# Kernel tuning notes

Measured on AMD Instinct MI355X. Metric: run time of the kernel, lower is better.

The kernel has to match this reference:

```python
import jax, jax.numpy as jnp
import numpy as np

ROPE_BASE = 100.0


def _rope1d(tok, pos):
    # tok: [B, H, N, d], pos: [B, N] int. Matches croco apply_rope1d.
    d = tok.shape[-1]
    inv_freq = 1.0 / (ROPE_BASE ** (jnp.arange(0, d, 2, dtype=jnp.float32) / d))  # [d/2]
    ang = pos[:, None, :, None].astype(jnp.float32) * inv_freq  # [B,1,N,d/2]
    ang = jnp.concatenate([ang, ang], axis=-1)  # [B,1,N,d]
    cos, sin = jnp.cos(ang).astype(tok.dtype), jnp.sin(ang).astype(tok.dtype)
    x1, x2 = tok[..., : d // 2], tok[..., d // 2 :]
    rot = jnp.concatenate([-x2, x1], axis=-1)  # rotate_half
    return tok * cos + rot * sin


def _rope2d(tok, pos):
    # tok: [B, H, N, D]; first half of D uses pos[...,0] (y), second half pos[...,1] (x)
    y, x = jnp.split(tok, 2, axis=-1)
    return jnp.concatenate([_rope1d(y, pos[..., 0]), _rope1d(x, pos[..., 1])], axis=-1)


def setup_inputs() -> dict:
    key = jax.random.key(0)
    ks = jax.random.split(key, 10)
    B, N, C = 8, 1024, 768
    s = 0.02
    return {
        "query": jax.random.normal(ks[0], (B, N, C), jnp.float32),
        "key": jax.random.normal(ks[1], (B, N, C), jnp.float32),
        "value": jax.random.normal(ks[2], (B, N, C), jnp.float32),
        "qpos": jax.random.randint(ks[3], (B, N, 2), 0, 32, jnp.int32),
        "kpos": jax.random.randint(ks[4], (B, N, 2), 0, 32, jnp.int32),
        "Wq": jax.random.normal(ks[5], (C, C), jnp.float32) * s,
        "Wk": jax.random.normal(ks[6], (C, C), jnp.float32) * s,
        "Wv": jax.random.normal(ks[7], (C, C), jnp.float32) * s,
        "Wo": jax.random.normal(ks[8], (C, C), jnp.float32) * s,
        "bo": jnp.zeros((C,), jnp.float32),
    }


def reference(query, key, value, qpos, kpos, Wq, Wk, Wv, Wo, bo):
    B, Nq, C = query.shape
    H = 12
    hd = C // H
    scale = hd ** -0.5
    # projections (torch Linear: x @ W^T), then split heads -> [B,H,N,hd]
    q = jnp.einsum("bnc,dc->bnd", query, Wq).reshape(B, Nq, H, hd).transpose(0, 2, 1, 3)
    k = jnp.einsum("bnc,dc->bnd", key, Wk).reshape(B, -1, H, hd).transpose(0, 2, 1, 3)
    v = jnp.einsum("bnc,dc->bnd", value, Wv).reshape(B, -1, H, hd).transpose(0, 2, 1, 3)
    q = _rope2d(q, qpos)
    k = _rope2d(k, kpos)
    attn = jnp.einsum("bhqd,bhkd->bhqk", q, k) * scale
    attn = jax.nn.softmax(attn, axis=-1)
    x = jnp.einsum("bhqk,bhkd->bhqd", attn, v)
    x = x.transpose(0, 2, 1, 3).reshape(B, Nq, C)
    return jnp.einsum("bnc,dc->bnd", x, Wo) + bo
```

## Files before the change

kernel.cpp:

```cpp
#include <hip/hip_runtime.h>
#include <hip/hip_bf16.h>
#include <hip/hip_fp16.h>

#define B_DIM 8
#define N_DIM 1024
#define C_DIM 768
#define H_DIM 12
#define HD    64
#define M_DIM (B_DIM * N_DIM)
#define BH    (B_DIM * H_DIM)

static constexpr size_t TEN = (size_t)M_DIM * C_DIM;
static constexpr size_t WN  = (size_t)C_DIM * C_DIM;

typedef __attribute__((ext_vector_type(8))) short    s16x8;
typedef __attribute__((ext_vector_type(8))) _Float16 f16x8;
typedef __attribute__((ext_vector_type(4))) float    f32x4;

__device__ __forceinline__ unsigned short f2h(float f) {
    __half h = __float2half(f);
    return __half_as_ushort(h);
}


__global__ __launch_bounds__(256)
void convX(const float* __restrict__ q, const float* __restrict__ k,
           const float* __restrict__ v, unsigned short* __restrict__ XS)
{
    const int t  = blockIdx.z;
    const int p  = blockIdx.y;
    const int kb = blockIdx.x;
    const float* src = (t == 0) ? q : (t == 1 ? k : v);
    unsigned short* dst = XS + (size_t)t * TEN;

    const int mr = threadIdx.x & 127;
    const int gh = threadIdx.x >> 7;
    const float* s = src + ((size_t)(p * 128 + mr)) * C_DIM + kb * 32 + gh * 16;
    float4 v0 = *(const float4*)(s);
    float4 v1 = *(const float4*)(s + 4);
    float4 v2 = *(const float4*)(s + 8);
    float4 v3 = *(const float4*)(s + 12);
    float f[16] = {v0.x,v0.y,v0.z,v0.w, v1.x,v1.y,v1.z,v1.w,
                   v2.x,v2.y,v2.z,v2.w, v3.x,v3.y,v3.z,v3.w};
    #pragma unroll
    for (int gj = 0; gj < 2; ++gj) {
        int gg = gh * 2 + gj;
        s16x8 h8;
        #pragma unroll
        for (int e = 0; e < 8; ++e)
            h8[e] = (short)f2h(f[gj * 8 + e]);
        size_t a = ((((size_t)p * 24 + kb) * 4 + gg) * 128 + mr) * 8;
        *(s16x8*)(dst + a) = h8;
    }
}

__global__ __launch_bounds__(256)
void convW(const float* __restrict__ wq, const float* __restrict__ wk,
           const float* __restrict__ wv, const float* __restrict__ wo,
           unsigned short* __restrict__ WS)
{
    const int t  = blockIdx.z;
    const int p  = blockIdx.y;
    const int kb = blockIdx.x;
    const float* src = (t == 0) ? wq : (t == 1 ? wk : (t == 2 ? wv : wo));
    unsigned short* dst = WS + (size_t)t * WN;

    const int mr = threadIdx.x & 127;
    const int gh = threadIdx.x >> 7;
    const float* s = src + ((size_t)(p * 128 + mr)) * C_DIM + kb * 32 + gh * 16;
    float4 v0 = *(const float4*)(s);
    float4 v1 = *(const float4*)(s + 4);
    float4 v2 = *(const float4*)(s + 8);
    float4 v3 = *(const float4*)(s + 12);
    float f[16] = {v0.x,v0.y,v0.z,v0.w, v1.x,v1.y,v1.z,v1.w,
                   v2.x,v2.y,v2.z,v2.w, v3.x,v3.y,v3.z,v3.w};
    #pragma unroll
    for (int gj = 0; gj < 2; ++gj) {
        int gg = gh * 2 + gj;
        s16x8 h8;
        #pragma unroll
        for (int e = 0; e < 8; ++e)
            h8[e] = (short)f2h(f[gj * 8 + e]);
        size_t a = ((((size_t)p * 24 + kb) * 4 + gg) * 128 + mr) * 8;
        *(s16x8*)(dst + a) = h8;
    }
}

__global__ void angles512(float2* __restrict__ tab)
{
    int t = threadIdx.x;
    int pos = t >> 4, j = t & 15;
    float ang = (float)pos * exp2f(-(float)j * 0.41524101186092029f);
    float s, c;
    sincosf(ang, &s, &c);
    tab[t] = make_float2(c, s);
}

template<int MODE>
__global__ __launch_bounds__(256)
void gemmF(const unsigned short* __restrict__ XQ, const unsigned short* __restrict__ XK,
           const unsigned short* __restrict__ XV,
           const unsigned short* __restrict__ WQ, const unsigned short* __restrict__ WK,
           const unsigned short* __restrict__ WV,
           const int* __restrict__ qpos, const int* __restrict__ kpos,
           const float2* __restrict__ tab,
           unsigned short* __restrict__ OQ, unsigned short* __restrict__ OK_,
           unsigned short* __restrict__ OV,
           const float* __restrict__ bias, float* __restrict__ Of)
{
    __shared__ unsigned short sA[3][4][128][8];
    __shared__ unsigned short sB[3][4][128][8];

    const int tid  = threadIdx.x;
    const int lane = tid & 63;
    const int w    = tid >> 6;
    const int wr   = w >> 1, wc = w & 1;
    const int c    = lane & 15, g = lane >> 4;

    const int chunk = gridDim.x >> 3;
    const int wgid  = (blockIdx.x & 7) * chunk + (blockIdx.x >> 3);
    int z, m0, n0;
    if (MODE == 1) {
        z = wgid / 384;
        int r = wgid - z * 384;
        m0 = (r / 6) * 128;
        n0 = (r % 6) * 128;
    } else {
        z = 0;
        m0 = (wgid / 6) * 128;
        n0 = (wgid % 6) * 128;
    }

    const unsigned short *Ap, *Bp;
    if (MODE == 0 || z == 0) { Ap = XQ; Bp = WQ; }
    else if (z == 1)         { Ap = XK; Bp = WK; }
    else                     { Ap = XV; Bp = WV; }

    const size_t abase0 = (size_t)(m0 >> 7) * 24 * 4096;
    const size_t bbase0 = (size_t)(n0 >> 7) * 24 * 4096;

    f32x4 acc[4][4] = {};

    auto stage = [&](int kb, int buf) {
        #pragma unroll
        for (int t = 0; t < 4; ++t) {
            int is = w * 4 + t;
            int sel = is >> 3;
            int j   = is & 7;
            int gg  = j >> 1, half = j & 1;
            const unsigned short* srcp =
                (sel ? Bp + bbase0 : Ap + abase0) + (size_t)kb * 4096
                + (size_t)gg * 1024 + (half * 64 + lane) * 8;
            unsigned short* dstp = sel ? &sB[buf][gg][half * 64][0]
                                       : &sA[buf][gg][half * 64][0];
            __builtin_amdgcn_global_load_lds(
                (const __attribute__((address_space(1))) void*)srcp,
                (__attribute__((address_space(3))) void*)dstp,
                16, 0, 0);
        }
    };

    stage(0, 0);
    stage(1, 1);
    stage(2, 2);

    for (int kb = 0; kb < 24; ++kb) {
        int buf = kb % 3;
        if (kb < 22)      asm volatile("s_waitcnt vmcnt(8)" ::: "memory");
        else if (kb == 22) asm volatile("s_waitcnt vmcnt(4)" ::: "memory");
        else               asm volatile("s_waitcnt vmcnt(0)" ::: "memory");
        __builtin_amdgcn_sched_barrier(0);
        __builtin_amdgcn_s_barrier();
        __builtin_amdgcn_sched_barrier(0);

        f16x8 a[4], b[4];
        #pragma unroll
        for (int mi = 0; mi < 4; ++mi)
            a[mi] = *(const f16x8*)&sA[buf][g][wr * 64 + 16 * mi + c][0];
        #pragma unroll
        for (int ni = 0; ni < 4; ++ni)
            b[ni] = *(const f16x8*)&sB[buf][g][wc * 64 + 16 * ni + c][0];
        __builtin_amdgcn_s_setprio(1);
        #pragma unroll
        for (int mi = 0; mi < 4; ++mi)
            #pragma unroll
            for (int ni = 0; ni < 4; ++ni)
                acc[mi][ni] = __builtin_amdgcn_mfma_f32_16x16x32_f16(a[mi], b[ni], acc[mi][ni], 0, 0, 0);
        __builtin_amdgcn_s_setprio(0);

        __builtin_amdgcn_sched_barrier(0);
        __builtin_amdgcn_s_barrier();
        __builtin_amdgcn_sched_barrier(0);
        if (kb + 3 < 24) stage(kb + 3, buf);
    }

    if (MODE == 0) {
        #pragma unroll
        for (int ni = 0; ni < 4; ++ni) {
            int d = n0 + wc * 64 + 16 * ni + c;
            float bv = bias[d];
            #pragma unroll
            for (int mi = 0; mi < 4; ++mi)
                #pragma unroll
                for (int r = 0; r < 4; ++r) {
                    int m = m0 + wr * 64 + 16 * mi + 4 * g + r;
                    Of[(size_t)m * C_DIM + d] = acc[mi][ni][r] + bv;
                }
        }
    } else if (z == 2) {
        #pragma unroll
        for (int ni = 0; ni < 4; ++ni) {
            int d = n0 + wc * 64 + 16 * ni + c;
            #pragma unroll
            for (int mi = 0; mi < 4; ++mi)
                #pragma unroll
                for (int r = 0; r < 4; ++r) {
                    int m = m0 + wr * 64 + 16 * mi + 4 * g + r;
                    OV[(size_t)m * C_DIM + d] = f2h(acc[mi][ni][r]);
                }
        }
    } else {
        const int* P = z ? kpos : qpos;
        unsigned short* T = z ? OK_ : OQ;
        const float scale = z ? 1.0f : 0.18033688011112042f;
        const int hh = (n0 >> 6) + wc;
        #pragma unroll
        for (int mi = 0; mi < 4; ++mi)
            #pragma unroll
            for (int r = 0; r < 4; ++r) {
                int m = m0 + wr * 64 + 16 * mi + 4 * g + r;
                int b = m >> 10, n = m & 1023;
                size_t base = ((size_t)(b * H_DIM + hh) * N_DIM + n) * HD;
                #pragma unroll
                for (int bb = 0; bb < 2; ++bb) {
                    int pos = P[2 * m + bb];
                    float2 cs = tab[pos * 16 + c];
                    float x1 = acc[mi][bb * 2 + 0][r];
                    float x2 = acc[mi][bb * 2 + 1][r];
                    float r1 = (x1 * cs.x - x2 * cs.y) * scale;
                    float r2 = (x2 * cs.x + x1 * cs.y) * scale;
                    T[base + bb * 32 + c]      = f2h(r1);
                    T[base + bb * 32 + 16 + c] = f2h(r2);
                }
            }
    }
}

__global__ __launch_bounds__(256)
void vtrans(const unsigned short* __restrict__ Vf, unsigned short* __restrict__ Vt)
{
    __shared__ unsigned short T[64][72];
    const int bh = blockIdx.y;
    const int nt = blockIdx.x;
    const int tid = threadIdx.x;
    const int b = bh / H_DIM, h = bh % H_DIM;
    const size_t hb = (size_t)bh * (N_DIM * HD);

    #pragma unroll
    for (int it = 0; it < 2; ++it) {
        int f = tid + it * 256;
        int r = f >> 3;
        int c8 = (f & 7) * 8;
        s16x8 v = *(const s16x8*)(Vf + ((size_t)(b * N_DIM + nt * 64 + r)) * C_DIM + h * HD + c8);
        #pragma unroll
        for (int j = 0; j < 8; ++j)
            T[c8 + j][r] = (unsigned short)v[j];
    }
    __syncthreads();
    #pragma unroll
    for (int it = 0; it < 2; ++it) {
        int f = tid + it * 256;
        int d = f >> 3;
        int nn = (f & 7) * 8;
        *(s16x8*)(Vt + hb + (size_t)d * N_DIM + nt * 64 + nn) = *(const s16x8*)&T[d][nn];
    }
}

__global__ __launch_bounds__(256)
void attn_f16(const unsigned short* __restrict__ Qh, const unsigned short* __restrict__ Kh,
              const unsigned short* __restrict__ Vt,
              unsigned short* __restrict__ Xb)
{
    __shared__ _Float16 sK[64][72];
    __shared__ _Float16 sV[64][72];
    __shared__ _Float16 sP[4][2][16][72];

    const int tid  = threadIdx.x;
    const int lane = tid & 63;
    const int wv   = tid >> 6;
    const int c    = lane & 15;
    const int g    = lane >> 4;

    const int bid   = blockIdx.x;
    const int xcd   = bid & 7;
    const int local = bid >> 3;
    const int bh    = xcd * 12 + (local >> 3);
    const int q0    = (local & 7) * 128;
    const size_t hb = (size_t)bh * (N_DIM * HD);

    const size_t qoffA = hb + (size_t)(q0 + wv * 32 + c) * HD;
    const size_t qoffB = qoffA + (size_t)16 * HD;
    f16x8 qA0 = *(const f16x8*)(Qh + qoffA + 8 * g);
    f16x8 qA1 = *(const f16x8*)(Qh + qoffA + 32 + 8 * g);
    f16x8 qB0 = *(const f16x8*)(Qh + qoffB + 8 * g);
    f16x8 qB1 = *(const f16x8*)(Qh + qoffB + 32 + 8 * g);

    f16x8 ones;
    #pragma unroll
    for (int e = 0; e < 8; ++e) ones[e] = (_Float16)1.0f;

    f32x4 accA[4] = {}, accB[4] = {};
    f32x4 lAcc[2] = {};

    const int f0 = tid, f1 = tid + 256;
    const int row0 = f0 >> 3, ch0 = (f0 & 7) * 8;
    const int row1 = f1 >> 3, ch1 = (f1 & 7) * 8;
    const unsigned short* Kbase = Kh + hb;
    const unsigned short* Vbase = Vt + hb;

    s16x8 rK0 = *(const s16x8*)(Kbase + (size_t)row0 * HD + ch0);
    s16x8 rK1 = *(const s16x8*)(Kbase + (size_t)row1 * HD + ch1);
    s16x8 rV0 = *(const s16x8*)(Vbase + (size_t)row0 * N_DIM + ch0);
    s16x8 rV1 = *(const s16x8*)(Vbase + (size_t)row1 * N_DIM + ch1);

    for (int kt = 0; kt < 16; ++kt) {
        __builtin_amdgcn_s_barrier();

        *(s16x8*)&sK[row0][ch0] = rK0;
        *(s16x8*)&sK[row1][ch1] = rK1;
        *(s16x8*)&sV[row0][ch0] = rV0;
        *(s16x8*)&sV[row1][ch1] = rV1;

        if (kt < 15) {
            rK0 = *(const s16x8*)(Kbase + (size_t)((kt + 1) * 64 + row0) * HD + ch0);
            rK1 = *(const s16x8*)(Kbase + (size_t)((kt + 1) * 64 + row1) * HD + ch1);
            rV0 = *(const s16x8*)(Vbase + (size_t)row0 * N_DIM + (kt + 1) * 64 + ch0);
            rV1 = *(const s16x8*)(Vbase + (size_t)row1 * N_DIM + (kt + 1) * 64 + ch1);
        }

        asm volatile("s_waitcnt lgkmcnt(0)" ::: "memory");
        __builtin_amdgcn_sched_barrier(0);
        __builtin_amdgcn_s_barrier();
        __builtin_amdgcn_sched_barrier(0);

        f32x4 sA[4] = {}, sB[4] = {};
        __builtin_amdgcn_s_setprio(1);
        #pragma unroll
        for (int st = 0; st < 4; ++st) {
            f16x8 a0 = *(const f16x8*)&sK[16 * st + c][8 * g];
            f16x8 a1 = *(const f16x8*)&sK[16 * st + c][32 + 8 * g];
            sA[st] = __builtin_amdgcn_mfma_f32_16x16x32_f16(a0, qA0, sA[st], 0, 0, 0);
            sA[st] = __builtin_amdgcn_mfma_f32_16x16x32_f16(a1, qA1, sA[st], 0, 0, 0);
            sB[st] = __builtin_amdgcn_mfma_f32_16x16x32_f16(a0, qB0, sB[st], 0, 0, 0);
            sB[st] = __builtin_amdgcn_mfma_f32_16x16x32_f16(a1, qB1, sB[st], 0, 0, 0);
        }
        __builtin_amdgcn_s_setprio(0);

        #pragma unroll
        for (int st = 0; st < 4; ++st) {
            float pA[4], pB[4];
            #pragma unroll
            for (int r = 0; r < 4; ++r) {
                pA[r] = __builtin_amdgcn_exp2f(sA[st][r]);
                pB[r] = __builtin_amdgcn_exp2f(sB[st][r]);
            }
            __half2 a01 = __float22half2_rn(make_float2(pA[0], pA[1]));
            __half2 a23 = __float22half2_rn(make_float2(pA[2], pA[3]));
            __half2 b01 = __float22half2_rn(make_float2(pB[0], pB[1]));
            __half2 b23 = __float22half2_rn(make_float2(pB[2], pB[3]));
            *(uint2*)&sP[wv][0][c][16 * st + 4 * g] =
                make_uint2(*(unsigned*)&a01, *(unsigned*)&a23);
            *(uint2*)&sP[wv][1][c][16 * st + 4 * g] =
                make_uint2(*(unsigned*)&b01, *(unsigned*)&b23);
        }

        __builtin_amdgcn_s_setprio(1);
        #pragma unroll
        for (int m = 0; m < 2; ++m) {
            f16x8 pbA = *(const f16x8*)&sP[wv][0][c][32 * m + 8 * g];
            f16x8 pbB = *(const f16x8*)&sP[wv][1][c][32 * m + 8 * g];
            #pragma unroll
            for (int sd = 0; sd < 4; ++sd) {
                f16x8 va = *(const f16x8*)&sV[16 * sd + c][32 * m + 8 * g];
                accA[sd] = __builtin_amdgcn_mfma_f32_16x16x32_f16(va, pbA, accA[sd], 0, 0, 0);
                accB[sd] = __builtin_amdgcn_mfma_f32_16x16x32_f16(va, pbB, accB[sd], 0, 0, 0);
            }
            lAcc[0] = __builtin_amdgcn_mfma_f32_16x16x32_f16(ones, pbA, lAcc[0], 0, 0, 0);
            lAcc[1] = __builtin_amdgcn_mfma_f32_16x16x32_f16(ones, pbB, lAcc[1], 0, 0, 0);
        }
        __builtin_amdgcn_s_setprio(0);
    }

    float invA = 1.0f / lAcc[0][0];
    float invB = 1.0f / lAcc[1][0];

    const int b = bh / H_DIM, h = bh % H_DIM;
    #pragma unroll
    for (int sub = 0; sub < 2; ++sub) {
        const f32x4* acc = sub ? accB : accA;
        float invl = sub ? invB : invA;
        const int q = q0 + wv * 32 + sub * 16 + c;
        const int m  = b * N_DIM + q;
        const int p_ = m >> 7, mr = m & 127;
        #pragma unroll
        for (int sd = 0; sd < 4; ++sd) {
            int kdim = h * 64 + 16 * sd + 4 * g;
            int kb = kdim >> 5;
            int gg = (kdim >> 3) & 3;
            int e  = kdim & 7;
            size_t a = ((((size_t)p_ * 24 + kb) * 4 + gg) * 128 + mr) * 8 + e;
            unsigned short hs[4];
            #pragma unroll
            for (int r = 0; r < 4; ++r)
                hs[r] = f2h(acc[sd][r] * invl);
            *(uint2*)(Xb + a) =
                make_uint2((unsigned)hs[0] | ((unsigned)hs[1] << 16),
                           (unsigned)hs[2] | ((unsigned)hs[3] << 16));
        }
    }
}

extern "C" void kernel_launch(void* const* d_in, const int* in_sizes, int n_in,
                              void* d_out, int out_size, void* d_ws, size_t ws_size,
                              hipStream_t stream)
{
    const float* query = (const float*)d_in[0];
    const float* key_  = (const float*)d_in[1];
    const float* value = (const float*)d_in[2];
    const int*   qpos  = (const int*)d_in[3];
    const int*   kpos  = (const int*)d_in[4];
    const float* Wq    = (const float*)d_in[5];
    const float* Wk    = (const float*)d_in[6];
    const float* Wv    = (const float*)d_in[7];
    const float* Wo    = (const float*)d_in[8];
    const float* bo    = (const float*)d_in[9];
    float* out = (float*)d_out;

    unsigned short* XS  = (unsigned short*)d_ws;
    unsigned short* WS  = XS + 3 * TEN;
    unsigned short* Qh  = WS + 4 * WN;
    unsigned short* Kh  = Qh + TEN;
    unsigned short* Vf  = Kh + TEN;
    unsigned short* Vt  = Vf + TEN;
    unsigned short* Xb  = Vt + TEN;
    float2* tab = (float2*)(Xb + TEN);

    angles512<<<1, 512, 0, stream>>>(tab);
    convX<<<dim3(24, 64, 3), 256, 0, stream>>>(query, key_, value, XS);
    convW<<<dim3(24, 6, 4), 256, 0, stream>>>(Wq, Wk, Wv, Wo, WS);

    gemmF<1><<<dim3(1152), 256, 0, stream>>>(
        XS + 0 * TEN, XS + 1 * TEN, XS + 2 * TEN,
        WS + 0 * WN, WS + 1 * WN, WS + 2 * WN,
        qpos, kpos, tab, Qh, Kh, Vf, nullptr, nullptr);

    vtrans<<<dim3(N_DIM / 64, BH), 256, 0, stream>>>(Vf, Vt);

    attn_f16<<<dim3(768), 256, 0, stream>>>(Qh, Kh, Vt, Xb);

    gemmF<0><<<dim3(384), 256, 0, stream>>>(
        Xb, nullptr, nullptr,
        WS + 3 * WN, nullptr, nullptr,
        nullptr, nullptr, nullptr, nullptr, nullptr, nullptr, bo, out);
}
```

Baseline: 145.9 us.

## Fuse V transpose into projection GEMM epilogue, merge angle table into convW

The V projection epilogue now stages the fp16 tile in shared memory and writes V directly in head-transposed [bh][d][n] layout. This removes the separate vtrans kernel and the round trip through the intermediate Vf buffer. The angle table is computed by the first block of convW, which drops one kernel launch. The GEMM pipeline goes from triple to double buffering with dynamic shared memory, reducing LDS use and possibly raising occupancy, at the cost of less latency hiding.

```diff
diff --git a/kernel.cpp b/kernel.cpp
--- a/kernel.cpp
+++ b/kernel.cpp
@@ -57,8 +57,20 @@
 __global__ __launch_bounds__(256)
 void convW(const float* __restrict__ wq, const float* __restrict__ wk,
            const float* __restrict__ wv, const float* __restrict__ wo,
-           unsigned short* __restrict__ WS)
+           unsigned short* __restrict__ WS, float2* __restrict__ tab)
 {
+    if (blockIdx.x == 0 && blockIdx.y == 0 && blockIdx.z == 0) {
+        #pragma unroll
+        for (int i = 0; i < 2; ++i) {
+            int t = threadIdx.x + i * 256;
+            int pos = t >> 4, j = t & 15;
+            float ang = (float)pos * exp2f(-(float)j * 0.41524101186092029f);
+            float s, c;
+            sincosf(ang, &s, &c);
+            tab[t] = make_float2(c, s);
+        }
+    }
+
     const int t  = blockIdx.z;
     const int p  = blockIdx.y;
     const int kb = blockIdx.x;
@@ -86,16 +98,6 @@
     }
 }
 
-__global__ void angles512(float2* __restrict__ tab)
-{
-    int t = threadIdx.x;
-    int pos = t >> 4, j = t & 15;
-    float ang = (float)pos * exp2f(-(float)j * 0.41524101186092029f);
-    float s, c;
-    sincosf(ang, &s, &c);
-    tab[t] = make_float2(c, s);
-}
-
 template<int MODE>
 __global__ __launch_bounds__(256)
 void gemmF(const unsigned short* __restrict__ XQ, const unsigned short* __restrict__ XK,
@@ -108,8 +110,9 @@
            unsigned short* __restrict__ OV,
            const float* __restrict__ bias, float* __restrict__ Of)
 {
-    __shared__ unsigned short sA[3][4][128][8];
-    __shared__ unsigned short sB[3][4][128][8];
+    extern __shared__ unsigned short smem_us[];
+    auto sA = reinterpret_cast<unsigned short (*)[4][128][8]>(smem_us);
+    auto sB = reinterpret_cast<unsigned short (*)[4][128][8]>(smem_us + 8192);
 
     const int tid  = threadIdx.x;
     const int lane = tid & 63;
@@ -162,13 +165,11 @@
 
     stage(0, 0);
     stage(1, 1);
-    stage(2, 2);
 
     for (int kb = 0; kb < 24; ++kb) {
-        int buf = kb % 3;
-        if (kb < 22)      asm volatile("s_waitcnt vmcnt(8)" ::: "memory");
-        else if (kb == 22) asm volatile("s_waitcnt vmcnt(4)" ::: "memory");
-        else               asm volatile("s_waitcnt vmcnt(0)" ::: "memory");
+        int buf = kb & 1;
+        if (kb < 23) asm volatile("s_waitcnt vmcnt(4)" ::: "memory");
+        else         asm volatile("s_waitcnt vmcnt(0)" ::: "memory");
         __builtin_amdgcn_sched_barrier(0);
         __builtin_amdgcn_s_barrier();
         __builtin_amdgcn_sched_barrier(0);
@@ -191,7 +192,7 @@
         __builtin_amdgcn_sched_barrier(0);
         __builtin_amdgcn_s_barrier();
         __builtin_amdgcn_sched_barrier(0);
-        if (kb + 3 < 24) stage(kb + 3, buf);
+        if (kb + 2 < 24) stage(kb + 2, buf);
     }
 
     if (MODE == 0) {
@@ -208,16 +209,33 @@
                 }
         }
     } else if (z == 2) {
+        __syncthreads();
+        auto T = reinterpret_cast<unsigned short (*)[132]>(smem_us);
         #pragma unroll
         for (int ni = 0; ni < 4; ++ni) {
-            int d = n0 + wc * 64 + 16 * ni + c;
-            #pragma unroll
-            for (int mi = 0; mi < 4; ++mi)
+            int dl = wc * 64 + 16 * ni + c;
+            #pragma unroll
+            for (int mi = 0; mi < 4; ++mi) {
+                int ml = wr * 64 + 16 * mi + 4 * g;
+                unsigned short hs[4];
                 #pragma unroll
-                for (int r = 0; r < 4; ++r) {
-                    int m = m0 + wr * 64 + 16 * mi + 4 * g + r;
-                    OV[(size_t)m * C_DIM + d] = f2h(acc[mi][ni][r]);
-                }
+                for (int r = 0; r < 4; ++r)
+                    hs[r] = f2h(acc[mi][ni][r]);
+                *(uint2*)&T[dl][ml] =
+                    make_uint2((unsigned)hs[0] | ((unsigned)hs[1] << 16),
+                               (unsigned)hs[2] | ((unsigned)hs[3] << 16));
+            }
+        }
+        __syncthreads();
+        const int b = m0 >> 10, nbase = m0 & 1023;
+        #pragma unroll
+        for (int it = 0; it < 8; ++it) {
+            int f  = tid + it * 256;
+            int dl = f >> 4;
+            int mc = (f & 15) * 8;
+            s16x8 vv = *(const s16x8*)&T[dl][mc];
+            int d = n0 + dl, h = d >> 6, dh = d & 63;
+            *(s16x8*)(OV + ((size_t)(b * H_DIM + h) * HD + dh) * N_DIM + nbase + mc) = vv;
         }
     } else {
         const int* P = z ? kpos : qpos;
@@ -247,36 +265,6 @@
 }
 
 __global__ __launch_bounds__(256)
-void vtrans(const unsigned short* __restrict__ Vf, unsigned short* __restrict__ Vt)
-{
-    __shared__ unsigned short T[64][72];
-    const int bh = blockIdx.y;
-    const int nt = blockIdx.x;
-    const int tid = threadIdx.x;
-    const int b = bh / H_DIM, h = bh % H_DIM;
-    const size_t hb = (size_t)bh * (N_DIM * HD);
-
-    #pragma unroll
-    for (int it = 0; it < 2; ++it) {
-        int f = tid + it * 256;
-        int r = f >> 3;
-        int c8 = (f & 7) * 8;
-        s16x8 v = *(const s16x8*)(Vf + ((size_t)(b * N_DIM + nt * 64 + r)) * C_DIM + h * HD + c8);
-        #pragma unroll
-        for (int j = 0; j < 8; ++j)
-            T[c8 + j][r] = (unsigned short)v[j];
-    }
-    __syncthreads();
-    #pragma unroll
-    for (int it = 0; it < 2; ++it) {
-        int f = tid + it * 256;
-        int d = f >> 3;
-        int nn = (f & 7) * 8;
-        *(s16x8*)(Vt + hb + (size_t)d * N_DIM + nt * 64 + nn) = *(const s16x8*)&T[d][nn];
-    }
-}
-
-__global__ __launch_bounds__(256)
 void attn_f16(const unsigned short* __restrict__ Qh, const unsigned short* __restrict__ Kh,
               const unsigned short* __restrict__ Vt,
               unsigned short* __restrict__ Xb)
@@ -440,25 +428,21 @@
     unsigned short* WS  = XS + 3 * TEN;
     unsigned short* Qh  = WS + 4 * WN;
     unsigned short* Kh  = Qh + TEN;
-    unsigned short* Vf  = Kh + TEN;
-    unsigned short* Vt  = Vf + TEN;
+    unsigned short* Vt  = Kh + TEN;
     unsigned short* Xb  = Vt + TEN;
     float2* tab = (float2*)(Xb + TEN);
 
-    angles512<<<1, 512, 0, stream>>>(tab);
     convX<<<dim3(24, 64, 3), 256, 0, stream>>>(query, key_, value, XS);
-    convW<<<dim3(24, 6, 4), 256, 0, stream>>>(Wq, Wk, Wv, Wo, WS);
-
-    gemmF<1><<<dim3(1152), 256, 0, stream>>>(
+    convW<<<dim3(24, 6, 4), 256, 0, stream>>>(Wq, Wk, Wv, Wo, WS, tab);
+
+    gemmF<1><<<dim3(1152), 256, 33792, stream>>>(
         XS + 0 * TEN, XS + 1 * TEN, XS + 2 * TEN,
         WS + 0 * WN, WS + 1 * WN, WS + 2 * WN,
-        qpos, kpos, tab, Qh, Kh, Vf, nullptr, nullptr);
-
-    vtrans<<<dim3(N_DIM / 64, BH), 256, 0, stream>>>(Vf, Vt);
+        qpos, kpos, tab, Qh, Kh, Vt, nullptr, nullptr);
 
     attn_f16<<<dim3(768), 256, 0, stream>>>(Qh, Kh, Vt, Xb);
 
-    gemmF<0><<<dim3(384), 256, 0, stream>>>(
+    gemmF<0><<<dim3(384), 256, 32768, stream>>>(
         Xb, nullptr, nullptr,
         WS + 3 * WN, nullptr, nullptr,
         nullptr, nullptr, nullptr, nullptr, nullptr, nullptr, bo, out);
```

Result: faster. 131.4 us (-10.0%).
